# Optimization experiments

Hardware: AMD Instinct MI355X
Metric: run time of the kernel (lower is better)

## Reference

```python
import jax, jax.numpy as jnp
import numpy as np

N, D, E, R, G, M = 8192, 1024, 64, 64, 8, 8

def setup_inputs() -> dict:
    key = jax.random.key(0)
    k_h, k_wg, k_wl, k_w1, k_w2 = jax.random.split(key, 5)
    return {
        'h': jax.random.normal(k_h, (N, D), jnp.float32),
        'Wg': jax.random.normal(k_wg, (D, G), jnp.float32) * 0.02,  # nn.Linear weight (transposed)
        'bg': jnp.zeros((G,), jnp.float32),
        'Wloc': jax.random.normal(k_wl, (G, D, M), jnp.float32) * 0.02,
        'W1': jax.random.normal(k_w1, (E, D, R), jnp.float32) * 0.02,
        'W2': jax.random.normal(k_w2, (E, R, D), jnp.float32) * 0.02,
        'k': 2,
    }

def reference(h, Wg, bg, Wloc, W1, W2, k):
    n, d = h.shape
    g, _, m = Wloc.shape
    e = W1.shape[0]
    router_temp = 1.0
    # stage 1: group routing (top-1)
    g_scores = h @ Wg + bg                                   # (N, G)
    group_idx = jnp.argmax(g_scores, axis=-1)                # (N,)
    # stage 2: within-group scores; compute all groups (cheap: N*G*M) then select
    all_local = jnp.einsum('nd,gdm->ngm', h, Wloc)           # (N, G, M)
    local_scores = jnp.take_along_axis(all_local, group_idx[:, None, None], axis=1)[:, 0]  # (N, M)
    topv, topm = jax.lax.top_k(local_scores, k)              # (N, k)
    gate = jax.nn.softmax(topv / max(router_temp, 1e-6), axis=-1)
    expert_ids = group_idx[:, None] * m + topm               # (N, k) global expert ids
    # scatter gates into dense (N, E); topm entries are distinct per token
    gate_full = jnp.zeros((n, e), h.dtype).at[jnp.arange(n)[:, None], expert_ids].set(gate)
    # low-rank expert compute: relu(h @ W1) @ W2, weighted-combined
    tmp = jax.nn.relu(jnp.einsum('nd,edr->ner', h, W1))      # (N, E, R)
    out = jnp.einsum('ner,erd->nd', gate_full[:, :, None] * tmp, W2)  # (N, D)
    return out, expert_ids, gate, group_idx
```

## Files before the change

kernel.cpp:

```cpp
#include <hip/hip_runtime.h>
#include <hip/hip_bf16.h>
#include <cstdint>
#include <cstddef>

#define NTOK 8192
#define DIM  1024
#define NEXP 64
#define RANK 64
#define NGRP 8
#define NLOC 8

typedef __attribute__((ext_vector_type(8))) short bf16x8;
typedef __attribute__((ext_vector_type(4))) float f32x4;

static __device__ inline unsigned int pack_bf16x2(float a, float b) {
    __hip_bfloat16 ha = __float2bfloat16(a);
    __hip_bfloat16 hb = __float2bfloat16(b);
    return (unsigned int)(*(unsigned short*)&ha) |
           ((unsigned int)(*(unsigned short*)&hb) << 16);
}

__global__ __launch_bounds__(512) void score_all(
    const float* __restrict__ h, const float* __restrict__ Wg,
    const float* __restrict__ Wloc, unsigned short* __restrict__ hb,
    float* __restrict__ Sp)
{
    __shared__ float Hs[128][66];
    __shared__ float Ws[40][72];

    const int tile = blockIdx.x;
    const int slab = blockIdx.y;
    const int z    = blockIdx.z;
    const int tid  = threadIdx.x;
    const int wave = tid >> 6;
    const int lane = tid & 63;
    const int t0   = tile * 128;
    const int kz   = z * 512;

    const int r0  = tid >> 2;
    const int seg = (tid & 3) * 16;

    float acc[10] = {};

    float4 hpre[4];
    float4 wgp;
    float4 wlp;

    {
        const int kb = kz;
        const float* src = h + (size_t)(t0 + r0) * DIM + kb + seg;
        hpre[0] = *(const float4*)(src);
        hpre[1] = *(const float4*)(src + 4);
        hpre[2] = *(const float4*)(src + 8);
        hpre[3] = *(const float4*)(src + 12);
        const int g = tid >> 7, r = tid & 127;
        if (slab == 0) {
            if (tid < 128)
                wgp = *(const float4*)(Wg + (size_t)(kb + (tid >> 1)) * NGRP + (tid & 1) * 4);
            wlp = *(const float4*)(Wloc + (size_t)g * (DIM * NLOC)
                                       + (size_t)(kb + (r >> 1)) * NLOC + (r & 1) * 4);
        } else {
            wlp = *(const float4*)(Wloc + (size_t)(4 + g) * (DIM * NLOC)
                                       + (size_t)(kb + (r >> 1)) * NLOC + (r & 1) * 4);
        }
    }

    for (int chunk = 0; chunk < 8; ++chunk) {
        const int kb = kz + chunk * 64;

        {
            float* dst = &Hs[r0][seg];
#pragma unroll
            for (int q = 0; q < 4; ++q) {
                const float4 v = hpre[q];
                *(float2*)(dst + q * 4)     = make_float2(v.x, v.y);
                *(float2*)(dst + q * 4 + 2) = make_float2(v.z, v.w);
            }
            if (slab == 0) {
                unsigned short* hrow = hb + (size_t)(t0 + r0) * DIM + kb + seg;
#pragma unroll
                for (int q = 0; q < 4; ++q) {
                    const float4 v = hpre[q];
                    uint2 pk;
                    pk.x = pack_bf16x2(v.x, v.y);
                    pk.y = pack_bf16x2(v.z, v.w);
                    *(uint2*)(hrow + q * 4) = pk;
                }
            }
        }
        {
            const int g = tid >> 7, r = tid & 127;
            const int k = r >> 1;
            if (slab == 0) {
                if (tid < 128) {
                    const int kk = tid >> 1, m4 = (tid & 1) * 4;
                    Ws[m4 + 0][kk] = wgp.x; Ws[m4 + 1][kk] = wgp.y;
                    Ws[m4 + 2][kk] = wgp.z; Ws[m4 + 3][kk] = wgp.w;
                }
                const int c = 8 + g * 8 + (r & 1) * 4;
                Ws[c + 0][k] = wlp.x; Ws[c + 1][k] = wlp.y;
                Ws[c + 2][k] = wlp.z; Ws[c + 3][k] = wlp.w;
            } else {
                const int c = g * 8 + (r & 1) * 4;
                Ws[c + 0][k] = wlp.x; Ws[c + 1][k] = wlp.y;
                Ws[c + 2][k] = wlp.z; Ws[c + 3][k] = wlp.w;
            }
        }
        __syncthreads();

        if (chunk < 7) {
            const int kbn = kb + 64;
            const float* src = h + (size_t)(t0 + r0) * DIM + kbn + seg;
            hpre[0] = *(const float4*)(src);
            hpre[1] = *(const float4*)(src + 4);
            hpre[2] = *(const float4*)(src + 8);
            hpre[3] = *(const float4*)(src + 12);
            const int g = tid >> 7, r = tid & 127;
            if (slab == 0) {
                if (tid < 128)
                    wgp = *(const float4*)(Wg + (size_t)(kbn + (tid >> 1)) * NGRP + (tid & 1) * 4);
                wlp = *(const float4*)(Wloc + (size_t)g * (DIM * NLOC)
                                           + (size_t)(kbn + (r >> 1)) * NLOC + (r & 1) * 4);
            } else {
                wlp = *(const float4*)(Wloc + (size_t)(4 + g) * (DIM * NLOC)
                                           + (size_t)(kbn + (r >> 1)) * NLOC + (r & 1) * 4);
            }
        }

        if (slab == 0) {
            const int c0 = wave * 5;
#pragma unroll 2
            for (int kq = 0; kq < 16; ++kq) {
                const int k0 = kq * 4;
                const float2 a00 = *(const float2*)&Hs[lane][k0];
                const float2 a01 = *(const float2*)&Hs[lane][k0 + 2];
                const float2 a10 = *(const float2*)&Hs[64 + lane][k0];
                const float2 a11 = *(const float2*)&Hs[64 + lane][k0 + 2];
                float4 bq[5];
#pragma unroll
                for (int c = 0; c < 5; ++c)
                    bq[c] = *(const float4*)&Ws[c0 + c][k0];
#pragma unroll
                for (int c = 0; c < 5; ++c) {
                    acc[c] += a00.x * bq[c].x; acc[5 + c] += a10.x * bq[c].x;
                }
#pragma unroll
                for (int c = 0; c < 5; ++c) {
                    acc[c] += a00.y * bq[c].y; acc[5 + c] += a10.y * bq[c].y;
                }
#pragma unroll
                for (int c = 0; c < 5; ++c) {
                    acc[c] += a01.x * bq[c].z; acc[5 + c] += a11.x * bq[c].z;
                }
#pragma unroll
                for (int c = 0; c < 5; ++c) {
                    acc[c] += a01.y * bq[c].w; acc[5 + c] += a11.y * bq[c].w;
                }
            }
        } else {
            const int c0 = wave * 4;
#pragma unroll 2
            for (int kq = 0; kq < 16; ++kq) {
                const int k0 = kq * 4;
                const float2 a00 = *(const float2*)&Hs[lane][k0];
                const float2 a01 = *(const float2*)&Hs[lane][k0 + 2];
                const float2 a10 = *(const float2*)&Hs[64 + lane][k0];
                const float2 a11 = *(const float2*)&Hs[64 + lane][k0 + 2];
                float4 bq[4];
#pragma unroll
                for (int c = 0; c < 4; ++c)
                    bq[c] = *(const float4*)&Ws[c0 + c][k0];
#pragma unroll
                for (int c = 0; c < 4; ++c) {
                    acc[c] += a00.x * bq[c].x; acc[5 + c] += a10.x * bq[c].x;
                }
#pragma unroll
                for (int c = 0; c < 4; ++c) {
                    acc[c] += a00.y * bq[c].y; acc[5 + c] += a10.y * bq[c].y;
                }
#pragma unroll
                for (int c = 0; c < 4; ++c) {
                    acc[c] += a01.x * bq[c].z; acc[5 + c] += a11.x * bq[c].z;
                }
#pragma unroll
                for (int c = 0; c < 4; ++c) {
                    acc[c] += a01.y * bq[c].w; acc[5 + c] += a11.y * bq[c].w;
                }
            }
        }
        __syncthreads();
    }

    const int gcol = (slab ? 40 + wave * 4 : wave * 5);
    const int nout = slab ? 4 : 5;
    float* dstS  = Sp + (size_t)z * (NTOK * 72) + (size_t)(t0 + lane) * 72 + gcol;
    float* dstS2 = Sp + (size_t)z * (NTOK * 72) + (size_t)(t0 + 64 + lane) * 72 + gcol;
#pragma unroll
    for (int c = 0; c < 5; ++c) {
        if (c < nout) {
            dstS[c]  = acc[c];
            dstS2[c] = acc[5 + c];
        }
    }
}

__global__ __launch_bounds__(256) void route_all(
    const float* __restrict__ Sp, const float* __restrict__ bg,
    float* __restrict__ out_gidx, float* __restrict__ out_eid,
    float* __restrict__ out_gate, int* __restrict__ ws_eids,
    float* __restrict__ ws_gates, int* __restrict__ counts_e)
{
    __shared__ int hist[NEXP];
    if (threadIdx.x < NEXP) hist[threadIdx.x] = 0;
    __syncthreads();

    const int t = blockIdx.x * 256 + threadIdx.x;
    const float* p0 = Sp + (size_t)t * 72;
    const float* p1 = p0 + (size_t)NTOK * 72;
    float s[72];
#pragma unroll
    for (int i = 0; i < 18; ++i) {
        const float4 a = *(const float4*)(p0 + i * 4);
        const float4 b = *(const float4*)(p1 + i * 4);
        s[i * 4 + 0] = a.x + b.x; s[i * 4 + 1] = a.y + b.y;
        s[i * 4 + 2] = a.z + b.z; s[i * 4 + 3] = a.w + b.w;
    }

    int gi = 0; float best = s[0] + bg[0];
#pragma unroll
    for (int g = 1; g < NGRP; ++g) {
        const float v = s[g] + bg[g];
        if (v > best) { best = v; gi = g; }
    }

    float ls[NLOC];
#pragma unroll
    for (int m = 0; m < NLOC; ++m) ls[m] = s[8 + gi * NLOC + m];

    int m1 = 0; float v1 = ls[0];
#pragma unroll
    for (int m = 1; m < NLOC; ++m) { if (ls[m] > v1) { v1 = ls[m]; m1 = m; } }
    int m2 = (m1 == 0) ? 1 : 0; float v2 = ls[m2];
#pragma unroll
    for (int m = 0; m < NLOC; ++m) {
        if (m != m1 && m != ((m1 == 0) ? 1 : 0) && ls[m] > v2) { v2 = ls[m]; m2 = m; }
    }
    const float e2v = expf(v2 - v1);
    const float inv = 1.f / (1.f + e2v);
    const float g0 = inv, g1 = e2v * inv;
    const int ea = gi * NLOC + m1, eb = gi * NLOC + m2;

    out_gidx[t] = (float)gi;
    out_eid[t * 2 + 0] = (float)ea;
    out_eid[t * 2 + 1] = (float)eb;
    out_gate[t * 2 + 0] = g0;
    out_gate[t * 2 + 1] = g1;
    ws_eids[t * 2 + 0] = ea;
    ws_eids[t * 2 + 1] = eb;
    ws_gates[t * 2 + 0] = g0;
    ws_gates[t * 2 + 1] = g1;
    atomicAdd(&hist[ea], 1);
    atomicAdd(&hist[eb], 1);

    __syncthreads();
    if (threadIdx.x < NEXP) atomicAdd(&counts_e[threadIdx.x], hist[threadIdx.x]);
}

__global__ __launch_bounds__(256) void scatter_e(
    const int* __restrict__ ws_eids, const float* __restrict__ ws_gates,
    const int* __restrict__ counts_e, int* __restrict__ cursor,
    int* __restrict__ token_list, float* __restrict__ slot_gate)
{
    __shared__ int offS[64];
    const int tid = threadIdx.x;
    if (tid < 64) {
        const int c = counts_e[tid];
        int s = c;
#pragma unroll
        for (int d = 1; d < 64; d <<= 1) {
            int v = __shfl_up(s, d, 64);
            if (tid >= d) s += v;
        }
        offS[tid] = s - c;
    }
    __syncthreads();
    const int t = blockIdx.x * 256 + tid;
    if (t >= NTOK) return;
#pragma unroll
    for (int j = 0; j < 2; ++j) {
        const int eid = ws_eids[t * 2 + j];
        const int pos = offS[eid] + atomicAdd(&cursor[eid], 1);
        token_list[pos] = t * 2 + j;
        slot_gate[pos] = ws_gates[t * 2 + j];
    }
}

__global__ __launch_bounds__(256) void prep_w(
    const float* __restrict__ W1, const float* __restrict__ W2,
    unsigned short* __restrict__ W1t, unsigned short* __restrict__ W2t)
{
    __shared__ float Ls[64][65];
    const int e = blockIdx.x;
    const int y = blockIdx.y;
    if (y < 16) {
        const int kb = y;
        const float* src = W1 + (size_t)e * DIM * RANK + (size_t)kb * 64 * RANK;
#pragma unroll
        for (int it = 0; it < 4; ++it) {
            const int kk = (threadIdx.x >> 4) + it * 16;
            const int rr = (threadIdx.x & 15) * 4;
            *(float4*)&Ls[kk][rr] = *(const float4*)(src + (size_t)kk * RANK + rr);
        }
        __syncthreads();
#pragma unroll
        for (int it = 0; it < 2; ++it) {
            const int idx = threadIdx.x + it * 256;
            const int r = idx >> 3, k8 = (idx & 7) * 8;
            uint4 v;
            v.x = pack_bf16x2(Ls[k8 + 0][r], Ls[k8 + 1][r]);
            v.y = pack_bf16x2(Ls[k8 + 2][r], Ls[k8 + 3][r]);
            v.z = pack_bf16x2(Ls[k8 + 4][r], Ls[k8 + 5][r]);
            v.w = pack_bf16x2(Ls[k8 + 6][r], Ls[k8 + 7][r]);
            *(uint4*)(W1t + (size_t)e * RANK * DIM + (size_t)r * DIM + kb * 64 + k8) = v;
        }
    } else {
        const int db = y - 16;
        const float* src = W2 + (size_t)e * RANK * DIM + db * 64;
#pragma unroll
        for (int it = 0; it < 4; ++it) {
            const int rr = (threadIdx.x >> 4) + it * 16;
            const int dd = (threadIdx.x & 15) * 4;
            *(float4*)&Ls[rr][dd] = *(const float4*)(src + (size_t)rr * DIM + dd);
        }
        __syncthreads();
#pragma unroll
        for (int it = 0; it < 2; ++it) {
            const int idx = threadIdx.x + it * 256;
            const int d = idx >> 3, r8 = (idx & 7) * 8;
            uint4 v;
            v.x = pack_bf16x2(Ls[r8 + 0][d], Ls[r8 + 1][d]);
            v.y = pack_bf16x2(Ls[r8 + 2][d], Ls[r8 + 3][d]);
            v.z = pack_bf16x2(Ls[r8 + 4][d], Ls[r8 + 5][d]);
            v.w = pack_bf16x2(Ls[r8 + 6][d], Ls[r8 + 7][d]);
            *(uint4*)(W2t + (size_t)e * DIM * RANK + (size_t)(db * 64 + d) * RANK + r8) = v;
        }
    }
}

__global__ __launch_bounds__(256, 2) void e1_mfma(
    const unsigned short* __restrict__ hb, const unsigned short* __restrict__ W1t,
    const int* __restrict__ counts_e, const int* __restrict__ token_list,
    const float* __restrict__ slot_gate, unsigned short* __restrict__ P)
{
    __shared__ unsigned short Hs[64 * 72];
    __shared__ unsigned short Ws[64 * 72];
    __shared__ int   tokS[64];
    __shared__ float gateS[64];
    __shared__ int   offS[65];

    const int e   = blockIdx.x;
    const int tid = threadIdx.x;
    if (tid < 64) {
        const int c = counts_e[tid];
        int s = c;
#pragma unroll
        for (int d = 1; d < 64; d <<= 1) {
            int v = __shfl_up(s, d, 64);
            if (tid >= d) s += v;
        }
        offS[tid] = s - c;
        if (tid == 63) offS[64] = s;
    }
    __syncthreads();
    const int n0 = offS[e];
    const int ne = offS[e + 1] - n0;

    const unsigned short* W1te = W1t + (size_t)e * RANK * DIM;
    const int wave = tid >> 6;
    const int lane = tid & 63;
    const int tx   = lane & 15;
    const int quad = lane >> 4;

    for (int tile = blockIdx.y; tile * 64 < ne; tile += 8) {
        const int row0 = tile * 64;
        __syncthreads();
        if (tid < 64) {
            const int gr = row0 + tid;
            tokS[tid]  = (gr < ne) ? token_list[n0 + gr] : -1;
            gateS[tid] = (gr < ne) ? slot_gate[n0 + gr] : 0.f;
        }
        f32x4 acc[4] = {};
        for (int kc = 0; kc < DIM; kc += 64) {
            __syncthreads();
#pragma unroll
            for (int it = 0; it < 2; ++it) {
                const int idx = tid + it * 256;
                const int s = idx >> 3, k8 = (idx & 7) * 8;
                const int ent = tokS[s];
                uint4 v = make_uint4(0, 0, 0, 0);
                if (ent >= 0)
                    v = *(const uint4*)(hb + (size_t)(ent >> 1) * DIM + kc + k8);
                *(uint4*)(Hs + s * 72 + k8) = v;
            }
#pragma unroll
            for (int it = 0; it < 2; ++it) {
                const int idx = tid + it * 256;
                const int r = idx >> 3, k8 = (idx & 7) * 8;
                *(uint4*)(Ws + r * 72 + k8) =
                    *(const uint4*)(W1te + (size_t)r * DIM + kc + k8);
            }
            __syncthreads();
#pragma unroll
            for (int ks = 0; ks < 2; ++ks) {
                const bf16x8 a = *(const bf16x8*)(Hs + (wave * 16 + tx) * 72 + ks * 32 + quad * 8);
#pragma unroll
                for (int j = 0; j < 4; ++j) {
                    const bf16x8 b = *(const bf16x8*)(Ws + (j * 16 + tx) * 72 + ks * 32 + quad * 8);
                    acc[j] = __builtin_amdgcn_mfma_f32_16x16x32_bf16(a, b, acc[j], 0, 0, 0);
                }
            }
        }
#pragma unroll
        for (int j = 0; j < 4; ++j) {
#pragma unroll
            for (int i = 0; i < 4; ++i) {
                const int sl = wave * 16 + quad * 4 + i;
                const int gr = row0 + sl;
                if (gr < ne) {
                    const float v = fmaxf(acc[j][i], 0.f) * gateS[sl];
                    __hip_bfloat16 hv = __float2bfloat16(v);
                    P[(size_t)(n0 + gr) * RANK + j * 16 + tx] = *(unsigned short*)&hv;
                }
            }
        }
    }
}

__global__ __launch_bounds__(256, 2) void e2_mfma(
    const unsigned short* __restrict__ P, const unsigned short* __restrict__ W2t,
    const int* __restrict__ counts_e, const int* __restrict__ token_list,
    float* __restrict__ out, float* __restrict__ contrib)
{
    __shared__ unsigned short Ps[64 * 72];
    __shared__ unsigned short W2s[64 * 72];
    __shared__ int tokS[64];
    __shared__ int offS[65];

    const int e = blockIdx.x;
    const int colbase = blockIdx.y * 64;
    const int tid = threadIdx.x;
    if (tid < 64) {
        const int c = counts_e[tid];
        int s = c;
#pragma unroll
        for (int d = 1; d < 64; d <<= 1) {
            int v = __shfl_up(s, d, 64);
            if (tid >= d) s += v;
        }
        offS[tid] = s - c;
        if (tid == 63) offS[64] = s;
    }
    __syncthreads();
    const int n0 = offS[e];
    const int ne = offS[e + 1] - n0;

    const unsigned short* W2te = W2t + (size_t)e * DIM * RANK;
    const int wave = tid >> 6;
    const int lane = tid & 63;
    const int tx   = lane & 15;
    const int quad = lane >> 4;

#pragma unroll
    for (int it = 0; it < 2; ++it) {
        const int idx = tid + it * 256;
        const int d = idx >> 3, r8 = (idx & 7) * 8;
        *(uint4*)(W2s + d * 72 + r8) =
            *(const uint4*)(W2te + (size_t)(colbase + d) * RANK + r8);
    }

    for (int tile = blockIdx.z; tile * 64 < ne; tile += 4) {
        const int row0 = tile * 64;
        __syncthreads();
        if (tid < 64) {
            const int gr = row0 + tid;
            tokS[tid] = (gr < ne) ? token_list[n0 + gr] : -1;
        }
#pragma unroll
        for (int it = 0; it < 2; ++it) {
            const int idx = tid + it * 256;
            const int s = idx >> 3, r8 = (idx & 7) * 8;
            const int gr = row0 + s;
            uint4 v = make_uint4(0, 0, 0, 0);
            if (gr < ne) v = *(const uint4*)(P + (size_t)(n0 + gr) * RANK + r8);
            *(uint4*)(Ps + s * 72 + r8) = v;
        }
        __syncthreads();
        f32x4 acc[4] = {};
#pragma unroll
        for (int ks = 0; ks < 2; ++ks) {
            const bf16x8 a = *(const bf16x8*)(Ps + (wave * 16 + tx) * 72 + ks * 32 + quad * 8);
#pragma unroll
            for (int j = 0; j < 4; ++j) {
                const bf16x8 b = *(const bf16x8*)(W2s + (j * 16 + tx) * 72 + ks * 32 + quad * 8);
                acc[j] = __builtin_amdgcn_mfma_f32_16x16x32_bf16(a, b, acc[j], 0, 0, 0);
            }
        }
#pragma unroll
        for (int i = 0; i < 4; ++i) {
            const int sl = wave * 16 + quad * 4 + i;
            const int ent = tokS[sl];
            if (ent >= 0) {
                float* base = (ent & 1) ? contrib : out;
                float* op = base + (size_t)(ent >> 1) * DIM + colbase;
#pragma unroll
                for (int j = 0; j < 4; ++j)
                    op[j * 16 + tx] = acc[j][i];
            }
        }
    }
}

__global__ __launch_bounds__(256) void combine_kernel(
    const float* __restrict__ contrib, float* __restrict__ out)
{
    const size_t i = (size_t)blockIdx.x * 256 + threadIdx.x;
    float4 a = ((const float4*)out)[i];
    const float4 b = ((const float4*)contrib)[i];
    a.x += b.x; a.y += b.y; a.z += b.z; a.w += b.w;
    ((float4*)out)[i] = a;
}

extern "C" void kernel_launch(void* const* d_in, const int* in_sizes, int n_in,
                              void* d_out, int out_size, void* d_ws, size_t ws_size,
                              hipStream_t stream)
{
    const float* h    = (const float*)d_in[0];
    const float* Wg   = (const float*)d_in[1];
    const float* bg   = (const float*)d_in[2];
    const float* Wloc = (const float*)d_in[3];
    const float* W1   = (const float*)d_in[4];
    const float* W2   = (const float*)d_in[5];

    float* out_f    = (float*)d_out;
    float* out_main = out_f;
    float* out_eid  = out_f + (size_t)NTOK * DIM;
    float* out_gate = out_eid + (size_t)NTOK * 2;
    float* out_gidx = out_gate + (size_t)NTOK * 2;

    int* ws_i        = (int*)d_ws;
    int* counts_e    = ws_i;
    int* cursor_e    = ws_i + 192;
    int* ws_eids     = ws_i + 16896;
    int* token_list  = ws_i + 33280;
    float* ws_f      = (float*)(ws_i + 49664);
    float* ws_gates  = ws_f;
    float* slot_gate = ws_f + 16384;
    float* Sp        = ws_f + 2 * 16384;
    unsigned short* P_h = (unsigned short*)(Sp + (size_t)2 * NTOK * 72);
    unsigned short* W1t = P_h + (size_t)16384 * RANK;
    unsigned short* W2t = W1t + (size_t)NEXP * RANK * DIM;
    float* contrib      = (float*)(W2t + (size_t)NEXP * DIM * RANK);
    unsigned short* hb = (unsigned short*)contrib;

    hipMemsetAsync(ws_i, 0, 256 * sizeof(int), stream);

    prep_w<<<dim3(NEXP, 32), 256, 0, stream>>>(W1, W2, W1t, W2t);
    score_all<<<dim3(64, 2, 2), 512, 0, stream>>>(h, Wg, Wloc, hb, Sp);
    route_all<<<NTOK / 256, 256, 0, stream>>>(Sp, bg, out_gidx, out_eid,
        out_gate, ws_eids, ws_gates, counts_e);
    scatter_e<<<NTOK / 256, 256, 0, stream>>>(ws_eids, ws_gates, counts_e,
        cursor_e, token_list, slot_gate);
    e1_mfma<<<dim3(NEXP, 8), 256, 0, stream>>>(hb, W1t, counts_e, token_list,
        slot_gate, P_h);
    e2_mfma<<<dim3(NEXP, 16, 4), 256, 0, stream>>>(P_h, W2t, counts_e, token_list,
        out_main, contrib);
    combine_kernel<<<(NTOK * DIM / 4) / 256, 256, 0, stream>>>(contrib, out_main);
}
```

Baseline: 254.5 us.

## Use fixed-capacity per-expert buckets and pre-transposed router weights

Removes the scatter kernel and the prefix-sum scans by having route_all append tokens directly into fixed-capacity per-expert buckets (ECAP=2048) via atomic cursors. The expert kernels index buckets by e*ECAP, and the cursor doubles as the count. Router weights are also pre-transposed into a contiguous Wt buffer in prep_w, so score_all reads weights straight from global memory instead of staging them through shared memory. Tokens beyond ECAP per expert are silently dropped, which could give wrong output under skewed routing. The global weight loads in the inner loop may also be slower than LDS reads.

```diff
diff --git a/kernel.cpp b/kernel.cpp
--- a/kernel.cpp
+++ b/kernel.cpp
@@ -9,6 +9,7 @@
 #define RANK 64
 #define NGRP 8
 #define NLOC 8
+#define ECAP 2048
 
 typedef __attribute__((ext_vector_type(8))) short bf16x8;
 typedef __attribute__((ext_vector_type(4))) float f32x4;
@@ -21,12 +22,10 @@
 }
 
 __global__ __launch_bounds__(512) void score_all(
-    const float* __restrict__ h, const float* __restrict__ Wg,
-    const float* __restrict__ Wloc, unsigned short* __restrict__ hb,
-    float* __restrict__ Sp)
+    const float* __restrict__ h, const float* __restrict__ Wt,
+    unsigned short* __restrict__ hb, float* __restrict__ Sp)
 {
     __shared__ float Hs[128][66];
-    __shared__ float Ws[40][72];
 
     const int tile = blockIdx.x;
     const int slab = blockIdx.y;
@@ -40,29 +39,18 @@
     const int r0  = tid >> 2;
     const int seg = (tid & 3) * 16;
 
+    const int c0g = slab ? (40 + wave * 4) : (wave * 5);
+    const float* wt0 = Wt + (size_t)c0g * 1024;
+
     float acc[10] = {};
 
     float4 hpre[4];
-    float4 wgp;
-    float4 wlp;
-
     {
-        const int kb = kz;
-        const float* src = h + (size_t)(t0 + r0) * DIM + kb + seg;
+        const float* src = h + (size_t)(t0 + r0) * DIM + kz + seg;
         hpre[0] = *(const float4*)(src);
         hpre[1] = *(const float4*)(src + 4);
         hpre[2] = *(const float4*)(src + 8);
         hpre[3] = *(const float4*)(src + 12);
-        const int g = tid >> 7, r = tid & 127;
-        if (slab == 0) {
-            if (tid < 128)
-                wgp = *(const float4*)(Wg + (size_t)(kb + (tid >> 1)) * NGRP + (tid & 1) * 4);
-            wlp = *(const float4*)(Wloc + (size_t)g * (DIM * NLOC)
-                                       + (size_t)(kb + (r >> 1)) * NLOC + (r & 1) * 4);
-        } else {
-            wlp = *(const float4*)(Wloc + (size_t)(4 + g) * (DIM * NLOC)
-                                       + (size_t)(kb + (r >> 1)) * NLOC + (r & 1) * 4);
-        }
     }
 
     for (int chunk = 0; chunk < 8; ++chunk) {
@@ -88,58 +76,29 @@
                 }
             }
         }
-        {
-            const int g = tid >> 7, r = tid & 127;
-            const int k = r >> 1;
-            if (slab == 0) {
-                if (tid < 128) {
-                    const int kk = tid >> 1, m4 = (tid & 1) * 4;
-                    Ws[m4 + 0][kk] = wgp.x; Ws[m4 + 1][kk] = wgp.y;
-                    Ws[m4 + 2][kk] = wgp.z; Ws[m4 + 3][kk] = wgp.w;
-                }
-                const int c = 8 + g * 8 + (r & 1) * 4;
-                Ws[c + 0][k] = wlp.x; Ws[c + 1][k] = wlp.y;
-                Ws[c + 2][k] = wlp.z; Ws[c + 3][k] = wlp.w;
-            } else {
-                const int c = g * 8 + (r & 1) * 4;
-                Ws[c + 0][k] = wlp.x; Ws[c + 1][k] = wlp.y;
-                Ws[c + 2][k] = wlp.z; Ws[c + 3][k] = wlp.w;
-            }
-        }
         __syncthreads();
 
         if (chunk < 7) {
-            const int kbn = kb + 64;
-            const float* src = h + (size_t)(t0 + r0) * DIM + kbn + seg;
+            const float* src = h + (size_t)(t0 + r0) * DIM + kb + 64 + seg;
             hpre[0] = *(const float4*)(src);
             hpre[1] = *(const float4*)(src + 4);
             hpre[2] = *(const float4*)(src + 8);
             hpre[3] = *(const float4*)(src + 12);
-            const int g = tid >> 7, r = tid & 127;
-            if (slab == 0) {
-                if (tid < 128)
-                    wgp = *(const float4*)(Wg + (size_t)(kbn + (tid >> 1)) * NGRP + (tid & 1) * 4);
-                wlp = *(const float4*)(Wloc + (size_t)g * (DIM * NLOC)
-                                           + (size_t)(kbn + (r >> 1)) * NLOC + (r & 1) * 4);
-            } else {
-                wlp = *(const float4*)(Wloc + (size_t)(4 + g) * (DIM * NLOC)
-                                           + (size_t)(kbn + (r >> 1)) * NLOC + (r & 1) * 4);
-            }
         }
 
         if (slab == 0) {
-            const int c0 = wave * 5;
-#pragma unroll 2
+#pragma unroll 4
             for (int kq = 0; kq < 16; ++kq) {
                 const int k0 = kq * 4;
+                const float* wtk = wt0 + kb + k0;
+                float4 bq[5];
+#pragma unroll
+                for (int c = 0; c < 5; ++c)
+                    bq[c] = *(const float4*)(wtk + (size_t)c * 1024);
                 const float2 a00 = *(const float2*)&Hs[lane][k0];
                 const float2 a01 = *(const float2*)&Hs[lane][k0 + 2];
                 const float2 a10 = *(const float2*)&Hs[64 + lane][k0];
                 const float2 a11 = *(const float2*)&Hs[64 + lane][k0 + 2];
-                float4 bq[5];
-#pragma unroll
-                for (int c = 0; c < 5; ++c)
-                    bq[c] = *(const float4*)&Ws[c0 + c][k0];
 #pragma unroll
                 for (int c = 0; c < 5; ++c) {
                     acc[c] += a00.x * bq[c].x; acc[5 + c] += a10.x * bq[c].x;
@@ -158,18 +117,18 @@
                 }
             }
         } else {
-            const int c0 = wave * 4;
-#pragma unroll 2
+#pragma unroll 4
             for (int kq = 0; kq < 16; ++kq) {
                 const int k0 = kq * 4;
+                const float* wtk = wt0 + kb + k0;
+                float4 bq[4];
+#pragma unroll
+                for (int c = 0; c < 4; ++c)
+                    bq[c] = *(const float4*)(wtk + (size_t)c * 1024);
                 const float2 a00 = *(const float2*)&Hs[lane][k0];
                 const float2 a01 = *(const float2*)&Hs[lane][k0 + 2];
                 const float2 a10 = *(const float2*)&Hs[64 + lane][k0];
                 const float2 a11 = *(const float2*)&Hs[64 + lane][k0 + 2];
-                float4 bq[4];
-#pragma unroll
-                for (int c = 0; c < 4; ++c)
-                    bq[c] = *(const float4*)&Ws[c0 + c][k0];
 #pragma unroll
                 for (int c = 0; c < 4; ++c) {
                     acc[c] += a00.x * bq[c].x; acc[5 + c] += a10.x * bq[c].x;
@@ -191,10 +150,9 @@
         __syncthreads();
     }
 
-    const int gcol = (slab ? 40 + wave * 4 : wave * 5);
     const int nout = slab ? 4 : 5;
-    float* dstS  = Sp + (size_t)z * (NTOK * 72) + (size_t)(t0 + lane) * 72 + gcol;
-    float* dstS2 = Sp + (size_t)z * (NTOK * 72) + (size_t)(t0 + 64 + lane) * 72 + gcol;
+    float* dstS  = Sp + (size_t)z * (NTOK * 72) + (size_t)(t0 + lane) * 72 + c0g;
+    float* dstS2 = Sp + (size_t)z * (NTOK * 72) + (size_t)(t0 + 64 + lane) * 72 + c0g;
 #pragma unroll
     for (int c = 0; c < 5; ++c) {
         if (c < nout) {
@@ -207,13 +165,9 @@
 __global__ __launch_bounds__(256) void route_all(
     const float* __restrict__ Sp, const float* __restrict__ bg,
     float* __restrict__ out_gidx, float* __restrict__ out_eid,
-    float* __restrict__ out_gate, int* __restrict__ ws_eids,
-    float* __restrict__ ws_gates, int* __restrict__ counts_e)
-{
-    __shared__ int hist[NEXP];
-    if (threadIdx.x < NEXP) hist[threadIdx.x] = 0;
-    __syncthreads();
-
+    float* __restrict__ out_gate, int* __restrict__ cursor,
+    int* __restrict__ token_list, float* __restrict__ slot_gate)
+{
     const int t = blockIdx.x * 256 + threadIdx.x;
     const float* p0 = Sp + (size_t)t * 72;
     const float* p1 = p0 + (size_t)NTOK * 72;
@@ -255,53 +209,42 @@
     out_eid[t * 2 + 1] = (float)eb;
     out_gate[t * 2 + 0] = g0;
     out_gate[t * 2 + 1] = g1;
-    ws_eids[t * 2 + 0] = ea;
-    ws_eids[t * 2 + 1] = eb;
-    ws_gates[t * 2 + 0] = g0;
-    ws_gates[t * 2 + 1] = g1;
-    atomicAdd(&hist[ea], 1);
-    atomicAdd(&hist[eb], 1);
-
-    __syncthreads();
-    if (threadIdx.x < NEXP) atomicAdd(&counts_e[threadIdx.x], hist[threadIdx.x]);
-}
-
-__global__ __launch_bounds__(256) void scatter_e(
-    const int* __restrict__ ws_eids, const float* __restrict__ ws_gates,
-    const int* __restrict__ counts_e, int* __restrict__ cursor,
-    int* __restrict__ token_list, float* __restrict__ slot_gate)
-{
-    __shared__ int offS[64];
-    const int tid = threadIdx.x;
-    if (tid < 64) {
-        const int c = counts_e[tid];
-        int s = c;
-#pragma unroll
-        for (int d = 1; d < 64; d <<= 1) {
-            int v = __shfl_up(s, d, 64);
-            if (tid >= d) s += v;
-        }
-        offS[tid] = s - c;
-    }
-    __syncthreads();
-    const int t = blockIdx.x * 256 + tid;
-    if (t >= NTOK) return;
-#pragma unroll
-    for (int j = 0; j < 2; ++j) {
-        const int eid = ws_eids[t * 2 + j];
-        const int pos = offS[eid] + atomicAdd(&cursor[eid], 1);
-        token_list[pos] = t * 2 + j;
-        slot_gate[pos] = ws_gates[t * 2 + j];
+
+    const int pA = atomicAdd(&cursor[ea], 1);
+    if (pA < ECAP) {
+        token_list[ea * ECAP + pA] = t * 2 + 0;
+        slot_gate[ea * ECAP + pA] = g0;
+    }
+    const int pB = atomicAdd(&cursor[eb], 1);
+    if (pB < ECAP) {
+        token_list[eb * ECAP + pB] = t * 2 + 1;
+        slot_gate[eb * ECAP + pB] = g1;
     }
 }
 
 __global__ __launch_bounds__(256) void prep_w(
     const float* __restrict__ W1, const float* __restrict__ W2,
-    unsigned short* __restrict__ W1t, unsigned short* __restrict__ W2t)
+    const float* __restrict__ Wg, const float* __restrict__ Wloc,
+    unsigned short* __restrict__ W1t, unsigned short* __restrict__ W2t,
+    float* __restrict__ Wt)
 {
     __shared__ float Ls[64][65];
     const int e = blockIdx.x;
     const int y = blockIdx.y;
+    if (y == 32) {
+        if (e < 36) {
+#pragma unroll
+            for (int cc = 0; cc < 2; ++cc) {
+                const int c = e * 2 + cc;
+                const float* src = (c < 8)
+                    ? (Wg + c)
+                    : (Wloc + (size_t)((c - 8) >> 3) * (DIM * NLOC) + ((c - 8) & 7));
+                for (int k = threadIdx.x; k < DIM; k += 256)
+                    Wt[(size_t)c * DIM + k] = src[(size_t)k * NLOC];
+            }
+        }
+        return;
+    }
     if (y < 16) {
         const int kb = y;
         const float* src = W1 + (size_t)e * DIM * RANK + (size_t)kb * 64 * RANK;
@@ -349,31 +292,18 @@
 
 __global__ __launch_bounds__(256, 2) void e1_mfma(
     const unsigned short* __restrict__ hb, const unsigned short* __restrict__ W1t,
-    const int* __restrict__ counts_e, const int* __restrict__ token_list,
+    const int* __restrict__ counts, const int* __restrict__ token_list,
     const float* __restrict__ slot_gate, unsigned short* __restrict__ P)
 {
     __shared__ unsigned short Hs[64 * 72];
     __shared__ unsigned short Ws[64 * 72];
     __shared__ int   tokS[64];
     __shared__ float gateS[64];
-    __shared__ int   offS[65];
 
     const int e   = blockIdx.x;
     const int tid = threadIdx.x;
-    if (tid < 64) {
-        const int c = counts_e[tid];
-        int s = c;
-#pragma unroll
-        for (int d = 1; d < 64; d <<= 1) {
-            int v = __shfl_up(s, d, 64);
-            if (tid >= d) s += v;
-        }
-        offS[tid] = s - c;
-        if (tid == 63) offS[64] = s;
-    }
-    __syncthreads();
-    const int n0 = offS[e];
-    const int ne = offS[e + 1] - n0;
+    const int ne  = min(counts[e], ECAP);
+    const int base = e * ECAP;
 
     const unsigned short* W1te = W1t + (size_t)e * RANK * DIM;
     const int wave = tid >> 6;
@@ -386,8 +316,8 @@
         __syncthreads();
         if (tid < 64) {
             const int gr = row0 + tid;
-            tokS[tid]  = (gr < ne) ? token_list[n0 + gr] : -1;
-            gateS[tid] = (gr < ne) ? slot_gate[n0 + gr] : 0.f;
+            tokS[tid]  = (gr < ne) ? token_list[base + gr] : -1;
+            gateS[tid] = (gr < ne) ? slot_gate[base + gr] : 0.f;
         }
         f32x4 acc[4] = {};
         for (int kc = 0; kc < DIM; kc += 64) {
@@ -429,7 +359,7 @@
                 if (gr < ne) {
                     const float v = fmaxf(acc[j][i], 0.f) * gateS[sl];
                     __hip_bfloat16 hv = __float2bfloat16(v);
-                    P[(size_t)(n0 + gr) * RANK + j * 16 + tx] = *(unsigned short*)&hv;
+                    P[(size_t)(base + gr) * RANK + j * 16 + tx] = *(unsigned short*)&hv;
                 }
             }
         }
@@ -438,31 +368,18 @@
 
 __global__ __launch_bounds__(256, 2) void e2_mfma(
     const unsigned short* __restrict__ P, const unsigned short* __restrict__ W2t,
-    const int* __restrict__ counts_e, const int* __restrict__ token_list,
+    const int* __restrict__ counts, const int* __restrict__ token_list,
     float* __restrict__ out, float* __restrict__ contrib)
 {
     __shared__ unsigned short Ps[64 * 72];
     __shared__ unsigned short W2s[64 * 72];
     __shared__ int tokS[64];
-    __shared__ int offS[65];
 
     const int e = blockIdx.x;
     const int colbase = blockIdx.y * 64;
     const int tid = threadIdx.x;
-    if (tid < 64) {
-        const int c = counts_e[tid];
-        int s = c;
-#pragma unroll
-        for (int d = 1; d < 64; d <<= 1) {
-            int v = __shfl_up(s, d, 64);
-            if (tid >= d) s += v;
-        }
-        offS[tid] = s - c;
-        if (tid == 63) offS[64] = s;
-    }
-    __syncthreads();
-    const int n0 = offS[e];
-    const int ne = offS[e + 1] - n0;
+    const int ne  = min(counts[e], ECAP);
+    const int base = e * ECAP;
 
     const unsigned short* W2te = W2t + (size_t)e * DIM * RANK;
     const int wave = tid >> 6;
@@ -483,7 +400,7 @@
         __syncthreads();
         if (tid < 64) {
             const int gr = row0 + tid;
-            tokS[tid] = (gr < ne) ? token_list[n0 + gr] : -1;
+            tokS[tid] = (gr < ne) ? token_list[base + gr] : -1;
         }
 #pragma unroll
         for (int it = 0; it < 2; ++it) {
@@ -491,7 +408,7 @@
             const int s = idx >> 3, r8 = (idx & 7) * 8;
             const int gr = row0 + s;
             uint4 v = make_uint4(0, 0, 0, 0);
-            if (gr < ne) v = *(const uint4*)(P + (size_t)(n0 + gr) * RANK + r8);
+            if (gr < ne) v = *(const uint4*)(P + (size_t)(base + gr) * RANK + r8);
             *(uint4*)(Ps + s * 72 + r8) = v;
         }
         __syncthreads();
@@ -510,8 +427,8 @@
             const int sl = wave * 16 + quad * 4 + i;
             const int ent = tokS[sl];
             if (ent >= 0) {
-                float* base = (ent & 1) ? contrib : out;
-                float* op = base + (size_t)(ent >> 1) * DIM + colbase;
+                float* basep = (ent & 1) ? contrib : out;
+                float* op = basep + (size_t)(ent >> 1) * DIM + colbase;
 #pragma unroll
                 for (int j = 0; j < 4; ++j)
                     op[j * 16 + tx] = acc[j][i];
@@ -548,31 +465,26 @@
     float* out_gidx = out_gate + (size_t)NTOK * 2;
 
     int* ws_i        = (int*)d_ws;
-    int* counts_e    = ws_i;
-    int* cursor_e    = ws_i + 192;
-    int* ws_eids     = ws_i + 16896;
-    int* token_list  = ws_i + 33280;
-    float* ws_f      = (float*)(ws_i + 49664);
-    float* ws_gates  = ws_f;
-    float* slot_gate = ws_f + 16384;
-    float* Sp        = ws_f + 2 * 16384;
-    unsigned short* P_h = (unsigned short*)(Sp + (size_t)2 * NTOK * 72);
-    unsigned short* W1t = P_h + (size_t)16384 * RANK;
+    int* cursor_e    = ws_i;
+    int* token_list  = ws_i + 1024;
+    float* slot_gate = (float*)(ws_i + 1024 + NEXP * ECAP);
+    float* Sp        = slot_gate + NEXP * ECAP;
+    float* Wt        = Sp + (size_t)2 * NTOK * 72;
+    unsigned short* P_h = (unsigned short*)(Wt + 72 * DIM);
+    unsigned short* W1t = P_h + (size_t)NEXP * ECAP * RANK;
     unsigned short* W2t = W1t + (size_t)NEXP * RANK * DIM;
     float* contrib      = (float*)(W2t + (size_t)NEXP * DIM * RANK);
     unsigned short* hb = (unsigned short*)contrib;
 
-    hipMemsetAsync(ws_i, 0, 256 * sizeof(int), stream);
-
-    prep_w<<<dim3(NEXP, 32), 256, 0, stream>>>(W1, W2, W1t, W2t);
-    score_all<<<dim3(64, 2, 2), 512, 0, stream>>>(h, Wg, Wloc, hb, Sp);
+    hipMemsetAsync(cursor_e, 0, 64 * sizeof(int), stream);
+
+    prep_w<<<dim3(NEXP, 33), 256, 0, stream>>>(W1, W2, Wg, Wloc, W1t, W2t, Wt);
+    score_all<<<dim3(64, 2, 2), 512, 0, stream>>>(h, Wt, hb, Sp);
     route_all<<<NTOK / 256, 256, 0, stream>>>(Sp, bg, out_gidx, out_eid,
-        out_gate, ws_eids, ws_gates, counts_e);
-    scatter_e<<<NTOK / 256, 256, 0, stream>>>(ws_eids, ws_gates, counts_e,
-        cursor_e, token_list, slot_gate);
-    e1_mfma<<<dim3(NEXP, 8), 256, 0, stream>>>(hb, W1t, counts_e, token_list,
+        out_gate, cursor_e, token_list, slot_gate);
+    e1_mfma<<<dim3(NEXP, 8), 256, 0, stream>>>(hb, W1t, cursor_e, token_list,
         slot_gate, P_h);
-    e2_mfma<<<dim3(NEXP, 16, 4), 256, 0, stream>>>(P_h, W2t, counts_e, token_list,
+    e2_mfma<<<dim3(NEXP, 16, 4), 256, 0, stream>>>(P_h, W2t, cursor_e, token_list,
         out_main, contrib);
     combine_kernel<<<(NTOK * DIM / 4) / 256, 256, 0, stream>>>(contrib, out_main);
 }
```

Result: slower. 266.5 us (+4.7%).
